# Kernel optimization log

Hardware: AMD Instinct MI355X
Metric: run time of the kernel (lower is better)

Reference implementation:

```python
import jax, jax.numpy as jnp
import numpy as np

LATENT = 128
HIDDEN = 512
N_STEPS = 50
BATCH = 8192


def _linear_init(k, fan_in, fan_out):
    kw, kb = jax.random.split(k)
    lim = 1.0 / np.sqrt(fan_in)
    W = jax.random.uniform(kw, (fan_in, fan_out), minval=-lim, maxval=lim, dtype=jnp.float32)
    b = jax.random.uniform(kb, (fan_out,), minval=-lim, maxval=lim, dtype=jnp.float32)
    return W, b


def setup_inputs() -> dict:
    key = jax.random.key(0)
    ks = jax.random.split(key, 6)
    in_dim = 2 * LATENT + 2  # x + condition + t_emb + target_emb
    W1, b1 = _linear_init(ks[0], in_dim, HIDDEN)
    W2, b2 = _linear_init(ks[1], HIDDEN, HIDDEN)
    W3, b3 = _linear_init(ks[2], HIDDEN, HIDDEN)
    W4, b4 = _linear_init(ks[3], HIDDEN, LATENT)
    condition = jax.random.normal(ks[4], (BATCH, LATENT), dtype=jnp.float32)
    x_init = jax.random.normal(ks[5], (BATCH, LATENT), dtype=jnp.float32)
    return dict(condition=condition, x_init=x_init,
                W1=W1, b1=b1, W2=W2, b2=b2, W3=W3, b3=b3, W4=W4, b4=b4,
                target_survival=1)


def reference(condition, x_init, W1, b1, W2, b2, W3, b3, W4, b4, target_survival):
    n_steps = N_STEPS
    betas = jnp.linspace(1e-4, 0.02, n_steps).astype(x_init.dtype)
    alphas = 1.0 - betas
    alphas_cumprod = jnp.cumprod(alphas)
    batch = condition.shape[0]
    # target = zeros if target_survival else ones (static python scalar)
    target = jnp.full((batch, 1), 0.0 if target_survival else 1.0, dtype=x_init.dtype)
    noise_key = jax.random.key(42)

    def step(x, t):
        t_emb = jnp.full((batch, 1), 1.0, x.dtype) * (t.astype(x.dtype) / n_steps)
        inp = jnp.concatenate([x, condition, t_emb, target], axis=-1)  # [B, 2L+2]
        h = jax.nn.gelu(inp @ W1 + b1, approximate=False)
        h = jax.nn.gelu(h @ W2 + b2, approximate=False)
        h = jax.nn.gelu(h @ W3 + b3, approximate=False)
        noise_pred = h @ W4 + b4  # [B, L]
        noise = jax.random.normal(jax.random.fold_in(noise_key, t), x.shape, x.dtype)
        noise = jnp.where(t > 0, noise, jnp.zeros_like(noise))  # no noise at t=0
        beta_t = betas[t]
        x = (x - beta_t / jnp.sqrt(1.0 - alphas_cumprod[t]) * noise_pred) / jnp.sqrt(alphas[t])
        x = x + jnp.sqrt(beta_t) * noise
        return x, None

    ts = jnp.arange(n_steps - 1, -1, -1)  # reversed(range(n_steps))
    x_final, _ = jax.lax.scan(step, x_init, ts)
    return x_final
```

## Files before the change

kernel.cpp:

```cpp
#include <hip/hip_runtime.h>
#include <stdint.h>
#include <stddef.h>


typedef __bf16 bf16;
typedef __bf16 bf16x4 __attribute__((ext_vector_type(4)));
typedef __bf16 bf16x8 __attribute__((ext_vector_type(8)));
typedef float  floatx4 __attribute__((ext_vector_type(4)));

#define NSTEPS    50
#define WG_ROWS   32
#define XB_STRIDE 136
#define H_STRIDE  520

__device__ __forceinline__ uint32_t rotl32(uint32_t x, int r) {
  return (x << r) | (x >> (32 - r));
}

__device__ __forceinline__ void threefry2x32(uint32_t k0, uint32_t k1,
                                             uint32_t x0, uint32_t x1,
                                             uint32_t& o0, uint32_t& o1) {
  uint32_t k2 = k0 ^ k1 ^ 0x1BD11BDAu;
  x0 += k0; x1 += k1;
#define TF_R(R) { x0 += x1; x1 = rotl32(x1, R); x1 ^= x0; }
  TF_R(13) TF_R(15) TF_R(26) TF_R(6)
  x0 += k1; x1 += k2 + 1u;
  TF_R(17) TF_R(29) TF_R(16) TF_R(24)
  x0 += k2; x1 += k0 + 2u;
  TF_R(13) TF_R(15) TF_R(26) TF_R(6)
  x0 += k0; x1 += k1 + 3u;
  TF_R(17) TF_R(29) TF_R(16) TF_R(24)
  x0 += k1; x1 += k2 + 4u;
  TF_R(13) TF_R(15) TF_R(26) TF_R(6)
  x0 += k2; x1 += k0 + 5u;
#undef TF_R
  o0 = x0; o1 = x1;
}

__device__ __forceinline__ float erfinv_xla_bl(float x) {
  float w = -0.6931471805599453f * __builtin_amdgcn_logf(fmaf(-x, x, 1.0f));
  float wa = w - 2.5f;
  float pa = 2.81022636e-08f;
  pa = fmaf(pa, wa, 3.43273939e-07f);
  pa = fmaf(pa, wa, -3.5233877e-06f);
  pa = fmaf(pa, wa, -4.39150654e-06f);
  pa = fmaf(pa, wa, 0.00021858087f);
  pa = fmaf(pa, wa, -0.00125372503f);
  pa = fmaf(pa, wa, -0.00417768164f);
  pa = fmaf(pa, wa, 0.246640727f);
  pa = fmaf(pa, wa, 1.50140941f);
  float wb = __builtin_amdgcn_sqrtf(w) - 3.0f;
  float pb = -0.000200214257f;
  pb = fmaf(pb, wb, 0.000100950558f);
  pb = fmaf(pb, wb, 0.00134934322f);
  pb = fmaf(pb, wb, -0.00367342844f);
  pb = fmaf(pb, wb, 0.00573950773f);
  pb = fmaf(pb, wb, -0.0076224613f);
  pb = fmaf(pb, wb, 0.00943887047f);
  pb = fmaf(pb, wb, 1.00167406f);
  pb = fmaf(pb, wb, 2.83297682f);
  float p = (w < 5.0f) ? pa : pb;
  return p * x;
}

__device__ __forceinline__ float gelu_fast(float x) {
  float z  = x * 0.7071067811865475f;
  float az = fabsf(z);
  float t  = __builtin_amdgcn_rcpf(fmaf(0.47047f, az, 1.0f));
  float p  = fmaf(0.7478556f, t, -0.0958798f);
  p = fmaf(p, t, 0.3480242f);
  float e  = __builtin_amdgcn_exp2f(az * az * -1.4426950408889634f);
  float te = t * e;
  float er = fmaf(-p, te, 1.0f);
  er = copysignf(er, z);
  float h = 0.5f * x;
  return fmaf(h, er, h);
}

template<int KSTEPS, int BSTRIDE, int UNROLL>
__device__ __forceinline__ void gemm2t(const bf16* __restrict__ h_lds,
                                       const bf16* __restrict__ A_pk,
                                       int lane, floatx4 (&acc)[2][2]) {
  const int nrow = lane & 15, q = lane >> 4;
  const bf16* b0 = h_lds + nrow * BSTRIDE + q * 8;
  const bf16* a0 = A_pk + lane * 8;
#pragma unroll UNROLL
  for (int ks = 0; ks < KSTEPS; ++ks) {
    bf16x8 bf0 = *(const bf16x8*)(b0 + ks * 32);
    bf16x8 bf1 = *(const bf16x8*)(b0 + 16 * BSTRIDE + ks * 32);
    bf16x8 aA  = *(const bf16x8*)(a0 + ks * 512);
    bf16x8 aB  = *(const bf16x8*)(a0 + (KSTEPS + ks) * 512);
    acc[0][0] = __builtin_amdgcn_mfma_f32_16x16x32_bf16(aA, bf0, acc[0][0], 0, 0, 0);
    acc[0][1] = __builtin_amdgcn_mfma_f32_16x16x32_bf16(aA, bf1, acc[0][1], 0, 0, 0);
    acc[1][0] = __builtin_amdgcn_mfma_f32_16x16x32_bf16(aB, bf0, acc[1][0], 0, 0, 0);
    acc[1][1] = __builtin_amdgcn_mfma_f32_16x16x32_bf16(aB, bf1, acc[1][1], 0, 0, 0);
  }
}

template<int KSTEPS, int BSTRIDE>
__device__ __forceinline__ void gemm1t(const bf16* __restrict__ h_lds,
                                       const bf16* __restrict__ A_pk,
                                       int lane, floatx4& acc) {
  const int nrow = lane & 15, q = lane >> 4;
  const bf16* b0 = h_lds + nrow * BSTRIDE + q * 8;
  const bf16* a0 = A_pk + lane * 8;
#pragma unroll 4
  for (int ks = 0; ks < KSTEPS; ++ks) {
    bf16x8 bfr = *(const bf16x8*)(b0 + ks * 32);
    bf16x8 af  = *(const bf16x8*)(a0 + ks * 512);
    acc = __builtin_amdgcn_mfma_f32_16x16x32_bf16(af, bfr, acc, 0, 0, 0);
  }
}

__global__ void diff_prep(const float* __restrict__ W1, const float* __restrict__ b1,
                          const float* __restrict__ W2, const float* __restrict__ W3,
                          const float* __restrict__ W4, const int* __restrict__ tsurv,
                          bf16* __restrict__ w1p, bf16* __restrict__ w1cp,
                          bf16* __restrict__ w2p, bf16* __restrict__ w3p,
                          bf16* __restrict__ w4p,
                          float* __restrict__ eb1, uint32_t* __restrict__ fk,
                          float* __restrict__ cst) {
  const int tid = blockIdx.x * blockDim.x + threadIdx.x;
  const int nth = gridDim.x * blockDim.x;
  for (int i = tid; i < 512 * 128; i += nth) {
    int j = i & 7, lane = (i >> 3) & 63, ks = (i >> 9) & 3, ntg = i >> 11;
    int n = ntg * 16 + (lane & 15);
    int k = ks * 32 + (lane >> 4) * 8 + j;
    w1p[i]  = (bf16)W1[k * 512 + n];
    w1cp[i] = (bf16)W1[(128 + k) * 512 + n];
  }
  for (int i = tid; i < 512 * 512; i += nth) {
    int j = i & 7, lane = (i >> 3) & 63, ks = (i >> 9) & 15, ntg = i >> 13;
    int n = ntg * 16 + (lane & 15);
    int k = ks * 32 + (lane >> 4) * 8 + j;
    w2p[i] = (bf16)W2[k * 512 + n];
    w3p[i] = (bf16)W3[k * 512 + n];
  }
  for (int i = tid; i < 128 * 512; i += nth) {
    int j = i & 7, lane = (i >> 3) & 63, ks = (i >> 9) & 15, ntg = i >> 13;
    int n = ntg * 16 + (lane & 15);
    int k = ks * 32 + (lane >> 4) * 8 + j;
    w4p[i] = (bf16)W4[k * 128 + n];
  }
  const float tgt = (tsurv[0] != 0) ? 0.0f : 1.0f;
  for (int i = tid; i < NSTEPS * 512; i += nth) {
    int t = i >> 9, n = i & 511;
    eb1[i] = b1[n] + ((float)t / 50.0f) * W1[256 * 512 + n] + tgt * W1[257 * 512 + n];
  }
  if (tid == 0) {
    float ac = 1.0f;
    for (int t = 0; t < NSTEPS; ++t) {
      float beta  = 1e-4f + (0.02f - 1e-4f) * ((float)t / 49.0f);
      float alpha = 1.0f - beta;
      ac *= alpha;
      cst[t]            = beta / sqrtf(1.0f - ac);
      cst[NSTEPS + t]   = 1.0f / sqrtf(alpha);
      cst[2*NSTEPS + t] = sqrtf(beta);
      uint32_t o0, o1;
      threefry2x32(0u, 42u, 0u, (uint32_t)t, o0, o1);
      fk[t] = o0; fk[NSTEPS + t] = o1;
    }
  }
}

__global__ __launch_bounds__(1024, 4) void diff_main(
    const float* __restrict__ cond, const float* __restrict__ xinit,
    const bf16* __restrict__ w1p, const bf16* __restrict__ w1cp,
    const bf16* __restrict__ w2p, const bf16* __restrict__ w3p,
    const bf16* __restrict__ w4p,
    const float* __restrict__ eb1, const float* __restrict__ b2,
    const float* __restrict__ b3, const float* __restrict__ b4,
    const uint32_t* __restrict__ fk, const float* __restrict__ cst,
    float* __restrict__ out) {
  __shared__ bf16 xb[WG_ROWS * XB_STRIDE];
  __shared__ bf16 hbA[WG_ROWS * H_STRIDE];
  __shared__ bf16 hbB[WG_ROWS * H_STRIDE];

  const int tid  = threadIdx.x;
  const int wave = tid >> 6;
  const int lane = tid & 63;
  const int nrow = lane & 15, q = lane >> 4;
  const int r0   = blockIdx.x * WG_ROWS;
  const int mc0  = wave * 32;
  const int qc   = q * 4;

  const int mtile4 = wave & 7;
  const int ntile4 = wave >> 3;
  const int n4     = ntile4 * 16 + nrow;
  const int xc0    = mtile4 * 16 + qc;

  {
    const int row = tid >> 5;
    const int c4  = (tid & 31) * 4;
    float4 a = *(const float4*)(xinit + (size_t)(r0 + row) * 128 + c4);
    float4 c = *(const float4*)(cond  + (size_t)(r0 + row) * 128 + c4);
    bf16x4 x4, c4v;
    x4[0] = (bf16)a.x; x4[1] = (bf16)a.y; x4[2] = (bf16)a.z; x4[3] = (bf16)a.w;
    c4v[0] = (bf16)c.x; c4v[1] = (bf16)c.y; c4v[2] = (bf16)c.z; c4v[3] = (bf16)c.w;
    *(bf16x4*)(xb  + row * XB_STRIDE + c4) = x4;
    *(bf16x4*)(hbA + row * H_STRIDE  + c4) = c4v;
  }
  float4 xreg = *(const float4*)(xinit + (size_t)(r0 + n4) * 128 + xc0);
  __syncthreads();

  floatx4 cpr[2][2] = {};
  gemm2t<4, H_STRIDE, 4>(hbA, w1cp + (wave * 2) * 4 * 512, lane, cpr);
  __syncthreads();

  for (int t = NSTEPS - 1; t >= 0; --t) {
    {
      floatx4 acc[2][2] = {};
      gemm2t<4, XB_STRIDE, 4>(xb, w1p + (wave * 2) * 4 * 512, lane, acc);
      const float* ebt = eb1 + t * 512;
#pragma unroll
      for (int mt = 0; mt < 2; ++mt) {
        const int col = mc0 + mt * 16 + qc;
        float4 bb = *(const float4*)(ebt + col);
#pragma unroll
        for (int nt = 0; nt < 2; ++nt) {
          bf16x4 g;
#pragma unroll
          for (int r = 0; r < 4; ++r)
            g[r] = (bf16)gelu_fast(acc[mt][nt][r] + cpr[mt][nt][r] + ((const float*)&bb)[r]);
          *(bf16x4*)(hbA + (nt * 16 + nrow) * H_STRIDE + col) = g;
        }
      }
    }
    __syncthreads();

    {
      floatx4 acc[2][2] = {};
      gemm2t<16, H_STRIDE, 4>(hbA, w2p + (wave * 2) * 16 * 512, lane, acc);
#pragma unroll
      for (int mt = 0; mt < 2; ++mt) {
        const int col = mc0 + mt * 16 + qc;
        float4 bb = *(const float4*)(b2 + col);
#pragma unroll
        for (int nt = 0; nt < 2; ++nt) {
          bf16x4 g;
#pragma unroll
          for (int r = 0; r < 4; ++r)
            g[r] = (bf16)gelu_fast(acc[mt][nt][r] + ((const float*)&bb)[r]);
          *(bf16x4*)(hbB + (nt * 16 + nrow) * H_STRIDE + col) = g;
        }
      }
    }
    __syncthreads();

    {
      floatx4 acc[2][2] = {};
      gemm2t<16, H_STRIDE, 4>(hbB, w3p + (wave * 2) * 16 * 512, lane, acc);
#pragma unroll
      for (int mt = 0; mt < 2; ++mt) {
        const int col = mc0 + mt * 16 + qc;
        float4 bb = *(const float4*)(b3 + col);
#pragma unroll
        for (int nt = 0; nt < 2; ++nt) {
          bf16x4 g;
#pragma unroll
          for (int r = 0; r < 4; ++r)
            g[r] = (bf16)gelu_fast(acc[mt][nt][r] + ((const float*)&bb)[r]);
          *(bf16x4*)(hbA + (nt * 16 + nrow) * H_STRIDE + col) = g;
        }
      }
    }
    __syncthreads();

    {
      floatx4 acc = {};
      gemm1t<16, H_STRIDE>(hbA + ntile4 * 16 * H_STRIDE,
                           w4p + mtile4 * 16 * 512, lane, acc);
      const float c1 = cst[t], c2 = cst[NSTEPS + t], c3 = cst[2 * NSTEPS + t];
      const uint32_t fk0 = fk[t], fk1 = fk[NSTEPS + t];
      const float zscale = (t > 0) ? 1.4142135381698608f * c3 : 0.0f;
      float4 bb = *(const float4*)(b4 + xc0);
      const uint32_t gbase = (uint32_t)(r0 + n4) * 128u + (uint32_t)xc0;
      bf16x4 xpk;
#pragma unroll
      for (int r = 0; r < 4; ++r) {
        float np = acc[r] + ((const float*)&bb)[r];
        uint32_t o0, o1;
        threefry2x32(fk0, fk1, 0u, gbase + (uint32_t)r, o0, o1);
        uint32_t bits = o0 ^ o1;
        float f01 = __uint_as_float((bits >> 9) | 0x3F800000u) - 1.0f;
        float u = fmaxf(-0.99999994f, fmaf(f01, 2.0f, -0.99999994f));
        float z = zscale * erfinv_xla_bl(u);
        float xn = (((float*)&xreg)[r] - c1 * np) * c2 + z;
        ((float*)&xreg)[r] = xn;
        xpk[r] = (bf16)xn;
      }
      *(bf16x4*)(xb + n4 * XB_STRIDE + xc0) = xpk;
    }
    __syncthreads();
  }

  *(float4*)(out + (size_t)(r0 + n4) * 128 + xc0) = xreg;
}

extern "C" void kernel_launch(void* const* d_in, const int* in_sizes, int n_in,
                              void* d_out, int out_size, void* d_ws, size_t ws_size,
                              hipStream_t stream) {
  const float* cond  = (const float*)d_in[0];
  const float* xinit = (const float*)d_in[1];
  const float* W1 = (const float*)d_in[2];
  const float* b1 = (const float*)d_in[3];
  const float* W2 = (const float*)d_in[4];
  const float* b2 = (const float*)d_in[5];
  const float* W3 = (const float*)d_in[6];
  const float* b3 = (const float*)d_in[7];
  const float* W4 = (const float*)d_in[8];
  const float* b4 = (const float*)d_in[9];
  const int* tsurv = (const int*)d_in[10];

  char* ws = (char*)d_ws;
  bf16* w1p  = (bf16*)(ws + 0);
  bf16* w1cp = (bf16*)(ws + 131072);
  bf16* w2p  = (bf16*)(ws + 262144);
  bf16* w3p  = (bf16*)(ws + 786432);
  bf16* w4p  = (bf16*)(ws + 1310720);
  float* eb1 = (float*)(ws + 1441792);
  uint32_t* fkp = (uint32_t*)(ws + 1544192);
  float* cstp = (float*)(ws + 1544704);

  diff_prep<<<1024, 256, 0, stream>>>(W1, b1, W2, W3, W4, tsurv,
                                      w1p, w1cp, w2p, w3p, w4p, eb1, fkp, cstp);
  diff_main<<<256, 1024, 0, stream>>>(cond, xinit, w1p, w1cp, w2p, w3p, w4p,
                                      eb1, b2, b3, b4, fkp, cstp, (float*)d_out);
}
```

Before: 985.3 us.

## Halve rows per workgroup and give each wave a 64-column by 16-row tile

Measured after the change: 1.538 ms. 1.56x slower.

```diff
diff --git a/kernel.cpp b/kernel.cpp
--- a/kernel.cpp
+++ b/kernel.cpp
@@ -9,7 +9,7 @@
 typedef float  floatx4 __attribute__((ext_vector_type(4)));
 
 #define NSTEPS    50
-#define WG_ROWS   32
+#define WG_ROWS   16
 #define XB_STRIDE 136
 #define H_STRIDE  520
 
@@ -77,38 +77,41 @@
   return fmaf(h, er, h);
 }
 
-template<int KSTEPS, int BSTRIDE, int UNROLL>
-__device__ __forceinline__ void gemm2t(const bf16* __restrict__ h_lds,
-                                       const bf16* __restrict__ A_pk,
-                                       int lane, floatx4 (&acc)[2][2]) {
-  const int nrow = lane & 15, q = lane >> 4;
-  const bf16* b0 = h_lds + nrow * BSTRIDE + q * 8;
-  const bf16* a0 = A_pk + lane * 8;
-#pragma unroll UNROLL
-  for (int ks = 0; ks < KSTEPS; ++ks) {
-    bf16x8 bf0 = *(const bf16x8*)(b0 + ks * 32);
-    bf16x8 bf1 = *(const bf16x8*)(b0 + 16 * BSTRIDE + ks * 32);
-    bf16x8 aA  = *(const bf16x8*)(a0 + ks * 512);
-    bf16x8 aB  = *(const bf16x8*)(a0 + (KSTEPS + ks) * 512);
-    acc[0][0] = __builtin_amdgcn_mfma_f32_16x16x32_bf16(aA, bf0, acc[0][0], 0, 0, 0);
-    acc[0][1] = __builtin_amdgcn_mfma_f32_16x16x32_bf16(aA, bf1, acc[0][1], 0, 0, 0);
-    acc[1][0] = __builtin_amdgcn_mfma_f32_16x16x32_bf16(aB, bf0, acc[1][0], 0, 0, 0);
-    acc[1][1] = __builtin_amdgcn_mfma_f32_16x16x32_bf16(aB, bf1, acc[1][1], 0, 0, 0);
-  }
-}
+#define MFMA16(a, b, c) __builtin_amdgcn_mfma_f32_16x16x32_bf16((a), (b), (c), 0, 0, 0)
 
 template<int KSTEPS, int BSTRIDE>
-__device__ __forceinline__ void gemm1t(const bf16* __restrict__ h_lds,
-                                       const bf16* __restrict__ A_pk,
-                                       int lane, floatx4& acc) {
+__device__ __forceinline__ void gemm4(const bf16* __restrict__ h_lds,
+                                      const bf16* __restrict__ A_pk,
+                                      int lane, floatx4 (&acc)[4]) {
   const int nrow = lane & 15, q = lane >> 4;
   const bf16* b0 = h_lds + nrow * BSTRIDE + q * 8;
   const bf16* a0 = A_pk + lane * 8;
 #pragma unroll 4
   for (int ks = 0; ks < KSTEPS; ++ks) {
-    bf16x8 bfr = *(const bf16x8*)(b0 + ks * 32);
-    bf16x8 af  = *(const bf16x8*)(a0 + ks * 512);
-    acc = __builtin_amdgcn_mfma_f32_16x16x32_bf16(af, bfr, acc, 0, 0, 0);
+    bf16x8 bf  = *(const bf16x8*)(b0 + ks * 32);
+    bf16x8 a0f = *(const bf16x8*)(a0 + (0 * KSTEPS + ks) * 512);
+    bf16x8 a1f = *(const bf16x8*)(a0 + (1 * KSTEPS + ks) * 512);
+    bf16x8 a2f = *(const bf16x8*)(a0 + (2 * KSTEPS + ks) * 512);
+    bf16x8 a3f = *(const bf16x8*)(a0 + (3 * KSTEPS + ks) * 512);
+    acc[0] = MFMA16(a0f, bf, acc[0]);
+    acc[1] = MFMA16(a1f, bf, acc[1]);
+    acc[2] = MFMA16(a2f, bf, acc[2]);
+    acc[3] = MFMA16(a3f, bf, acc[3]);
+  }
+}
+
+template<int BSTRIDE>
+__device__ __forceinline__ void gemm_l4(const bf16* __restrict__ h_lds,
+                                        const bf16* __restrict__ A_pk,
+                                        int lane, floatx4& acc) {
+  const int nrow = lane & 15, q = lane >> 4;
+  const bf16* b0 = h_lds + nrow * BSTRIDE + q * 8;
+  const bf16* a0 = A_pk + lane * 8;
+#pragma unroll 4
+  for (int ks = 0; ks < 16; ++ks) {
+    bf16x8 bf = *(const bf16x8*)(b0 + ks * 32);
+    bf16x8 af = *(const bf16x8*)(a0 + ks * 512);
+    acc = MFMA16(af, bf, acc);
   }
 }
 
@@ -163,7 +166,7 @@
   }
 }
 
-__global__ __launch_bounds__(1024, 4) void diff_main(
+__global__ __launch_bounds__(512, 4) void diff_main(
     const float* __restrict__ cond, const float* __restrict__ xinit,
     const bf16* __restrict__ w1p, const bf16* __restrict__ w1cp,
     const bf16* __restrict__ w2p, const bf16* __restrict__ w3p,
@@ -181,13 +184,15 @@
   const int lane = tid & 63;
   const int nrow = lane & 15, q = lane >> 4;
   const int r0   = blockIdx.x * WG_ROWS;
-  const int mc0  = wave * 32;
+  const int mc0  = wave * 64;
   const int qc   = q * 4;
-
-  const int mtile4 = wave & 7;
-  const int ntile4 = wave >> 3;
-  const int n4     = ntile4 * 16 + nrow;
-  const int xc0    = mtile4 * 16 + qc;
+  const int xc0  = wave * 16 + qc;
+
+  const bf16* w1base  = w1p  + (wave * 4) * 4  * 512;
+  const bf16* w1cbase = w1cp + (wave * 4) * 4  * 512;
+  const bf16* w2base  = w2p  + (wave * 4) * 16 * 512;
+  const bf16* w3base  = w3p  + (wave * 4) * 16 * 512;
+  const bf16* w4base  = w4p  + wave * 16 * 512;
 
   {
     const int row = tid >> 5;
@@ -200,81 +205,71 @@
     *(bf16x4*)(xb  + row * XB_STRIDE + c4) = x4;
     *(bf16x4*)(hbA + row * H_STRIDE  + c4) = c4v;
   }
-  float4 xreg = *(const float4*)(xinit + (size_t)(r0 + n4) * 128 + xc0);
+  float4 xreg = *(const float4*)(xinit + (size_t)(r0 + nrow) * 128 + xc0);
   __syncthreads();
 
-  floatx4 cpr[2][2] = {};
-  gemm2t<4, H_STRIDE, 4>(hbA, w1cp + (wave * 2) * 4 * 512, lane, cpr);
+  floatx4 cpr[4] = {};
+  gemm4<4, H_STRIDE>(hbA, w1cbase, lane, cpr);
   __syncthreads();
 
   for (int t = NSTEPS - 1; t >= 0; --t) {
     {
-      floatx4 acc[2][2] = {};
-      gemm2t<4, XB_STRIDE, 4>(xb, w1p + (wave * 2) * 4 * 512, lane, acc);
+      floatx4 acc[4] = {};
+      gemm4<4, XB_STRIDE>(xb, w1base, lane, acc);
       const float* ebt = eb1 + t * 512;
 #pragma unroll
-      for (int mt = 0; mt < 2; ++mt) {
+      for (int mt = 0; mt < 4; ++mt) {
         const int col = mc0 + mt * 16 + qc;
         float4 bb = *(const float4*)(ebt + col);
-#pragma unroll
-        for (int nt = 0; nt < 2; ++nt) {
-          bf16x4 g;
-#pragma unroll
-          for (int r = 0; r < 4; ++r)
-            g[r] = (bf16)gelu_fast(acc[mt][nt][r] + cpr[mt][nt][r] + ((const float*)&bb)[r]);
-          *(bf16x4*)(hbA + (nt * 16 + nrow) * H_STRIDE + col) = g;
-        }
+        bf16x4 g;
+#pragma unroll
+        for (int r = 0; r < 4; ++r)
+          g[r] = (bf16)gelu_fast(acc[mt][r] + cpr[mt][r] + ((const float*)&bb)[r]);
+        *(bf16x4*)(hbA + nrow * H_STRIDE + col) = g;
       }
     }
     __syncthreads();
 
     {
-      floatx4 acc[2][2] = {};
-      gemm2t<16, H_STRIDE, 4>(hbA, w2p + (wave * 2) * 16 * 512, lane, acc);
-#pragma unroll
-      for (int mt = 0; mt < 2; ++mt) {
+      floatx4 acc[4] = {};
+      gemm4<16, H_STRIDE>(hbA, w2base, lane, acc);
+#pragma unroll
+      for (int mt = 0; mt < 4; ++mt) {
         const int col = mc0 + mt * 16 + qc;
         float4 bb = *(const float4*)(b2 + col);
-#pragma unroll
-        for (int nt = 0; nt < 2; ++nt) {
-          bf16x4 g;
-#pragma unroll
-          for (int r = 0; r < 4; ++r)
-            g[r] = (bf16)gelu_fast(acc[mt][nt][r] + ((const float*)&bb)[r]);
-          *(bf16x4*)(hbB + (nt * 16 + nrow) * H_STRIDE + col) = g;
-        }
+        bf16x4 g;
+#pragma unroll
+        for (int r = 0; r < 4; ++r)
+          g[r] = (bf16)gelu_fast(acc[mt][r] + ((const float*)&bb)[r]);
+        *(bf16x4*)(hbB + nrow * H_STRIDE + col) = g;
       }
     }
     __syncthreads();
 
     {
-      floatx4 acc[2][2] = {};
-      gemm2t<16, H_STRIDE, 4>(hbB, w3p + (wave * 2) * 16 * 512, lane, acc);
-#pragma unroll
-      for (int mt = 0; mt < 2; ++mt) {
+      floatx4 acc[4] = {};
+      gemm4<16, H_STRIDE>(hbB, w3base, lane, acc);
+#pragma unroll
+      for (int mt = 0; mt < 4; ++mt) {
         const int col = mc0 + mt * 16 + qc;
         float4 bb = *(const float4*)(b3 + col);
-#pragma unroll
-        for (int nt = 0; nt < 2; ++nt) {
-          bf16x4 g;
-#pragma unroll
-          for (int r = 0; r < 4; ++r)
-            g[r] = (bf16)gelu_fast(acc[mt][nt][r] + ((const float*)&bb)[r]);
-          *(bf16x4*)(hbA + (nt * 16 + nrow) * H_STRIDE + col) = g;
-        }
+        bf16x4 g;
+#pragma unroll
+        for (int r = 0; r < 4; ++r)
+          g[r] = (bf16)gelu_fast(acc[mt][r] + ((const float*)&bb)[r]);
+        *(bf16x4*)(hbA + nrow * H_STRIDE + col) = g;
       }
     }
     __syncthreads();
 
     {
       floatx4 acc = {};
-      gemm1t<16, H_STRIDE>(hbA + ntile4 * 16 * H_STRIDE,
-                           w4p + mtile4 * 16 * 512, lane, acc);
+      gemm_l4<H_STRIDE>(hbA, w4base, lane, acc);
       const float c1 = cst[t], c2 = cst[NSTEPS + t], c3 = cst[2 * NSTEPS + t];
       const uint32_t fk0 = fk[t], fk1 = fk[NSTEPS + t];
       const float zscale = (t > 0) ? 1.4142135381698608f * c3 : 0.0f;
       float4 bb = *(const float4*)(b4 + xc0);
-      const uint32_t gbase = (uint32_t)(r0 + n4) * 128u + (uint32_t)xc0;
+      const uint32_t gbase = (uint32_t)(r0 + nrow) * 128u + (uint32_t)xc0;
       bf16x4 xpk;
 #pragma unroll
       for (int r = 0; r < 4; ++r) {
@@ -289,12 +284,12 @@
         ((float*)&xreg)[r] = xn;
         xpk[r] = (bf16)xn;
       }
-      *(bf16x4*)(xb + n4 * XB_STRIDE + xc0) = xpk;
+      *(bf16x4*)(xb + nrow * XB_STRIDE + xc0) = xpk;
     }
     __syncthreads();
   }
 
-  *(float4*)(out + (size_t)(r0 + n4) * 128 + xc0) = xreg;
+  *(float4*)(out + (size_t)(r0 + nrow) * 128 + xc0) = xreg;
 }
 
 extern "C" void kernel_launch(void* const* d_in, const int* in_sizes, int n_in,
@@ -324,6 +319,6 @@
 
   diff_prep<<<1024, 256, 0, stream>>>(W1, b1, W2, W3, W4, tsurv,
                                       w1p, w1cp, w2p, w3p, w4p, eb1, fkp, cstp);
-  diff_main<<<256, 1024, 0, stream>>>(cond, xinit, w1p, w1cp, w2p, w3p, w4p,
-                                      eb1, b2, b3, b4, fkp, cstp, (float*)d_out);
-}
+  diff_main<<<512, 512, 0, stream>>>(cond, xinit, w1p, w1cp, w2p, w3p, w4p,
+                                     eb1, b2, b3, b4, fkp, cstp, (float*)d_out);
+}
```
